# Kernel tuning notes

Hardware: AMD Instinct MI355X
Metric: run time of the kernel (lower is better)

Reference implementation:

```python
import jax, jax.numpy as jnp
import numpy as np
import math

D_MODEL = 1024
NHEAD = 16
D_K = D_MODEL // NHEAD
LAMDA_ATT = 1.0
B, L = 2, 2048


def setup_inputs() -> dict:
    key = jax.random.key(0)
    ks = jax.random.split(key, 10)
    s = 1.0 / math.sqrt(D_MODEL)
    x = jax.random.normal(ks[0], (B, L, D_MODEL), dtype=jnp.float32)
    delta_r = jax.random.uniform(ks[1], (B, L), dtype=jnp.float32)  # positive, fed to log
    Wq = jax.random.normal(ks[2], (D_MODEL, D_MODEL), dtype=jnp.float32) * s
    Wk = jax.random.normal(ks[3], (D_MODEL, D_MODEL), dtype=jnp.float32) * s
    Wv = jax.random.normal(ks[4], (D_MODEL, D_MODEL), dtype=jnp.float32) * s
    Wo = jax.random.normal(ks[5], (D_MODEL, D_MODEL), dtype=jnp.float32) * s
    bq = jnp.zeros((D_MODEL,), jnp.float32)
    bk = jnp.zeros((D_MODEL,), jnp.float32)
    bv = jnp.zeros((D_MODEL,), jnp.float32)
    bo = jnp.zeros((D_MODEL,), jnp.float32)
    return {"x": x, "delta_r": delta_r, "Wq": Wq, "bq": bq, "Wk": Wk, "bk": bk,
            "Wv": Wv, "bv": bv, "Wo": Wo, "bo": bo}


def reference(x, delta_r, Wq, bq, Wk, bk, Wv, bv, Wo, bo):
    b, l, d = x.shape
    h, dk = NHEAD, D_K

    def proj(y, W, bias):
        # [B,L,D] -> [B,H,L,dk]
        return (y @ W + bias).reshape(b, l, h, dk).transpose(0, 2, 1, 3)

    v_scaled = x * delta_r[..., None]
    q = proj(x, Wq, bq)
    k = proj(x, Wk, bk)
    v = proj(v_scaled, Wv, bv)

    scores = jnp.einsum('bhqd,bhkd->bhqk', q, k) / math.sqrt(dk)
    pos = jnp.arange(l)
    dist = jnp.abs(pos[None, :] - pos[:, None]).astype(scores.dtype)  # [L,L]
    rel_bias = LAMDA_ATT * jnp.log(delta_r + 1e-6)  # [B,L]
    scores = scores - dist[None, None] * 0.1 + rel_bias[:, None, None, :]

    attn = jax.nn.softmax(scores, axis=-1)  # dropout is identity in eval mode
    context = jnp.einsum('bhqk,bhkd->bqhd', attn, v).reshape(b, l, d)
    out = context @ Wo + bo
    return out, attn.mean(axis=1)
```

## Files before the change

### kernel.cpp

```cpp
#include <hip/hip_runtime.h>
#include <math.h>

#define DMODEL 1024
#define NHEAD  16
#define DK     64
#define BB     2
#define LL     2048
#define MTOT   (BB*LL)

#define LOG2E      1.4426950408889634f
#define SCQ        (0.125f * LOG2E)
#define C2LOG      (0.1f * LOG2E)
#define SKIP_BOUND (-24.0f)

typedef __bf16 bf16_t;
typedef __bf16 bf16x8 __attribute__((ext_vector_type(8)));
typedef __bf16 bf16x4 __attribute__((ext_vector_type(4)));
typedef float  f32x4  __attribute__((ext_vector_type(4)));

static __device__ __forceinline__ f32x4 mfma16(bf16x8 a, bf16x8 b, f32x4 c) {
    return __builtin_amdgcn_mfma_f32_16x16x32_bf16(a, b, c, 0, 0, 0);
}
static __device__ __forceinline__ float exp2f_fast(float x) {
    return __builtin_amdgcn_exp2f(x);
}
static __device__ __forceinline__ float log2f_fast(float x) {
    return __builtin_amdgcn_logf(x);
}
static __device__ __forceinline__ void gl_lds16(const bf16_t* g, bf16_t* l) {
    __builtin_amdgcn_global_load_lds(
        (const __attribute__((address_space(1))) unsigned int*)g,
        (__attribute__((address_space(3))) unsigned int*)l, 16, 0, 0);
}

__global__ __launch_bounds__(256) void prep_fused_k(
    const float* __restrict__ x, const float* __restrict__ dr,
    bf16_t* __restrict__ xb, float* __restrict__ logd2,
    const float* __restrict__ Wq, const float* __restrict__ Wk,
    const float* __restrict__ Wv, const float* __restrict__ Wo,
    bf16_t* __restrict__ Wcat, bf16_t* __restrict__ Wot)
{
    __shared__ __align__(16) float Ts[64][68];
    const int bid = blockIdx.x;
    const int tid = threadIdx.x;
    if (bid < 2048) {
        size_t gid = (size_t)bid * 256 + tid;
        size_t off = gid * 8;
        float4 a = *(const float4*)(x + off);
        float4 c = *(const float4*)(x + off + 4);
        float va[8] = {a.x, a.y, a.z, a.w, c.x, c.y, c.z, c.w};
        bf16x8 o1;
#pragma unroll
        for (int j = 0; j < 8; ++j) o1[j] = (bf16_t)va[j];
        *(bf16x8*)(xb + off) = o1;
        if (gid < MTOT) logd2[gid] = log2f_fast(dr[gid] + 1e-6f);
    } else {
        const int t = bid - 2048;
        const int z = t >> 8;
        const float* W = (z == 0) ? Wq : (z == 1) ? Wk : (z == 2) ? Wv : Wo;
        bf16_t* dst = (z < 3) ? (Wcat + (size_t)z * DMODEL * DMODEL) : Wot;
        const int k0 = (t & 15) * 64, n0 = ((t >> 4) & 15) * 64;
#pragma unroll
        for (int i = 0; i < 4; ++i) {
            int u = tid + 256 * i, r = u >> 4, c4 = (u & 15) * 4;
            *(float4*)&Ts[r][c4] = *(const float4*)(W + (size_t)(k0 + r) * DMODEL + n0 + c4);
        }
        __syncthreads();
#pragma unroll
        for (int i = 0; i < 2; ++i) {
            int u = tid + 256 * i, n = u >> 3, k8 = (u & 7) * 8;
            bf16x8 v;
#pragma unroll
            for (int j = 0; j < 8; ++j) v[j] = (bf16_t)Ts[k8 + j][n];
            *(bf16x8*)(dst + (size_t)(n0 + n) * DMODEL + k0 + k8) = v;
        }
    }
}

__global__ __launch_bounds__(256, 3) void gemm128_k(
    const bf16_t* __restrict__ A, const bf16_t* __restrict__ Bt,
    const float* __restrict__ b0, const float* __restrict__ b1,
    const float* __restrict__ b2, const float* __restrict__ delta,
    float* __restrict__ outf, bf16_t* __restrict__ outQ,
    bf16_t* __restrict__ outK, bf16_t* __restrict__ outVt, int mode)
{
    __shared__ __align__(16) bf16_t Asw[128 * 64];
    __shared__ __align__(16) bf16_t Bsw[128 * 64];
    const int tid = threadIdx.x, lane = tid & 63, w = tid >> 6;
    const int quad = lane >> 4, n16 = lane & 15;
    const int wm = (w & 1) * 64, wn = (w >> 1) * 64;
    const int m0 = blockIdx.y * 128, n0 = blockIdx.x * 128;
    const int srow = lane >> 3;
    const int scb  = (lane & 7) ^ srow;

    f32x4 acc[4][4] = {};

    for (int K0 = 0; K0 < DMODEL; K0 += 64) {
        __syncthreads();
#pragma unroll
        for (int i = 0; i < 4; ++i) {
            int rb = w * 32 + i * 8;
            gl_lds16(A  + (size_t)(m0 + rb + srow) * DMODEL + K0 + scb * 8,
                     &Asw[rb * 64]);
            gl_lds16(Bt + (size_t)(n0 + rb + srow) * DMODEL + K0 + scb * 8,
                     &Bsw[rb * 64]);
        }
        __syncthreads();
#pragma unroll
        for (int kc = 0; kc < 2; ++kc) {
            const int pcb = ((kc * 4 + quad) ^ (n16 & 7)) * 8;
            bf16x8 af[4], bfv[4];
#pragma unroll
            for (int mi = 0; mi < 4; ++mi)
                af[mi] = *(const bf16x8*)&Asw[(wm + mi * 16 + n16) * 64 + pcb];
#pragma unroll
            for (int ni = 0; ni < 4; ++ni)
                bfv[ni] = *(const bf16x8*)&Bsw[(wn + ni * 16 + n16) * 64 + pcb];
#pragma unroll
            for (int mi = 0; mi < 4; ++mi)
#pragma unroll
                for (int ni = 0; ni < 4; ++ni)
                    acc[mi][ni] = mfma16(af[mi], bfv[ni], acc[mi][ni]);
        }
    }

    if (mode == 0) {
        const int region = n0 >> 10;
        if (region == 2) {
#pragma unroll
            for (int mi = 0; mi < 4; ++mi) {
                const int mbase = m0 + wm + mi * 16 + quad * 4;
                const int bidx = mbase >> 11, l = mbase & (LL - 1);
                const f32x4 dm4 = *(const f32x4*)(delta + mbase);
#pragma unroll
                for (int ni = 0; ni < 4; ++ni) {
                    const int nl = (n0 & 1023) + wn + ni * 16 + n16;
                    const int h = nl >> 6, dd = nl & 63;
                    const float bv = b2[nl];
                    bf16x4 pk;
#pragma unroll
                    for (int r = 0; r < 4; ++r)
                        pk[r] = (bf16_t)(acc[mi][ni][r] * dm4[r] + bv);
                    *(bf16x4*)(outVt + ((size_t)(bidx * NHEAD + h) * DK + dd) * LL + l) = pk;
                }
            }
        } else {
            const float* bias = (region == 0) ? b0 : b1;
            bf16_t* dst = (region == 0) ? outQ : outK;
            const float qs = (region == 0) ? SCQ : 1.0f;
#pragma unroll
            for (int mi = 0; mi < 4; ++mi) {
#pragma unroll
                for (int r = 0; r < 4; ++r) {
                    const int m = m0 + wm + mi * 16 + quad * 4 + r;
                    const int bidx = m >> 11, l = m & (LL - 1);
#pragma unroll
                    for (int ni = 0; ni < 4; ++ni) {
                        const int nl = (n0 & 1023) + wn + ni * 16 + n16;
                        const int h = nl >> 6, dd = nl & 63;
                        float v = (acc[mi][ni][r] + bias[nl]) * qs;
                        dst[(((size_t)(bidx * NHEAD + h) * LL) + l) * DK + dd] = (bf16_t)v;
                    }
                }
            }
        }
    } else {
#pragma unroll
        for (int mi = 0; mi < 4; ++mi) {
#pragma unroll
            for (int r = 0; r < 4; ++r) {
                const int m = m0 + wm + mi * 16 + quad * 4 + r;
#pragma unroll
                for (int ni = 0; ni < 4; ++ni) {
                    const int n = n0 + wn + ni * 16 + n16;
                    outf[(size_t)m * DMODEL + n] = acc[mi][ni][r] + b0[n];
                }
            }
        }
    }
}

__global__ __launch_bounds__(256) void stats_k(
    const bf16_t* __restrict__ Q, const bf16_t* __restrict__ K,
    const float* __restrict__ logd2, float* __restrict__ Qn,
    float* __restrict__ Kn, float* __restrict__ dlb, float* __restrict__ ldx)
{
    __shared__ float qn_s[2048], kn_s[2048], dg_s[2048];
    const int tid = threadIdx.x, bh = blockIdx.x, b = bh >> 4;
    const size_t base = (size_t)bh * LL * DK;
#pragma unroll
    for (int i = 0; i < 8; ++i) {
        const int row = tid + 256 * i;
        float qn2 = 0.f, kn2 = 0.f, dg = 0.f;
#pragma unroll
        for (int j = 0; j < 8; ++j) {
            bf16x8 qv = *(const bf16x8*)(Q + base + (size_t)row * DK + j * 8);
            bf16x8 kv = *(const bf16x8*)(K + base + (size_t)row * DK + j * 8);
#pragma unroll
            for (int e = 0; e < 8; ++e) {
                float fq = (float)qv[e], fk = (float)kv[e];
                qn2 += fq * fq; kn2 += fk * fk; dg += fq * fk;
            }
        }
        qn_s[row] = qn2;
        kn_s[row] = kn2;
        dg_s[row] = dg + logd2[b * LL + row];
    }
    __syncthreads();
    if (tid < 16) {
        float mq = 0.f, md = 1e30f;
        for (int r = 0; r < 128; ++r) {
            mq = fmaxf(mq, qn_s[tid * 128 + r]);
            md = fminf(md, dg_s[tid * 128 + r]);
        }
        Qn[bh * 16 + tid] = sqrtf(mq);
        dlb[bh * 16 + tid] = md;
    } else if (tid >= 64 && tid < 96) {
        const int t = tid - 64;
        float mk = 0.f;
        for (int r = 0; r < 64; ++r) mk = fmaxf(mk, kn_s[t * 64 + r]);
        Kn[bh * 32 + t] = sqrtf(mk);
    } else if (tid >= 128 && tid < 160 && (bh & 15) == 0) {
        const int t = tid - 128;
        float ml = -1e30f;
        for (int r = 0; r < 64; ++r) ml = fmaxf(ml, logd2[b * LL + t * 64 + r]);
        ldx[b * 32 + t] = ml;
    }
}

__global__ __launch_bounds__(256) void mlstat_k(
    const float* __restrict__ mlws, float* __restrict__ mlmin)
{
    __shared__ float s[2048];
    const int tid = threadIdx.x, bh = blockIdx.x;
#pragma unroll
    for (int i = 0; i < 8; ++i)
        s[tid + 256 * i] = mlws[(size_t)bh * LL + tid + 256 * i];
    __syncthreads();
    if (tid < 16) {
        float m = 1e30f;
        for (int r = 0; r < 128; ++r) m = fminf(m, s[tid * 128 + r]);
        mlmin[bh * 16 + tid] = m;
    }
}

__global__ __launch_bounds__(256, 4) void attn_flash_mfma_k(
    const bf16_t* __restrict__ Q, const bf16_t* __restrict__ K,
    const bf16_t* __restrict__ Vt, const float* __restrict__ logd2,
    const float* __restrict__ Qn, const float* __restrict__ Kn,
    const float* __restrict__ dlb, const float* __restrict__ ldx,
    bf16_t* __restrict__ ctx, float* __restrict__ mlout)
{
    __shared__ __align__(16) bf16_t Ks[64][72];
    __shared__ __align__(16) bf16_t Vts[64][72];
    __shared__ __align__(16) bf16_t Ps[4][16][72];
    __shared__ float logds[64];

    const int tid = threadIdx.x;
    const int lane = tid & 63, w = tid >> 6;
    const int quad = lane >> 4, n16 = lane & 15;
    const int bh = blockIdx.x, b = bh >> 4, h = bh & 15;
    const int qt = blockIdx.y, q0 = qt * 64;
    const size_t base = (size_t)bh * LL * DK;
    const int q = q0 + w * 16 + n16;

    bf16x8 qa[2];
#pragma unroll
    for (int kc = 0; kc < 2; ++kc)
        qa[kc] = *(const bf16x8*)(Q + base + (size_t)q * DK + kc * 32 + quad * 8);

    unsigned mask = 0;
    {
        const float qn = Qn[bh * 16 + (qt >> 1)], dl = dlb[bh * 16 + (qt >> 1)];
        for (int t = 0; t < 32; ++t) {
            const int kc0 = t * 64;
            const int dmin = (kc0 > q0 + 63) ? (kc0 - (q0 + 63))
                           : ((q0 > kc0 + 63) ? (q0 - (kc0 + 63)) : 0);
            const float bound = qn * Kn[bh * 32 + t] + ldx[b * 32 + t]
                              - C2LOG * (float)dmin - dl;
            if (bound > SKIP_BOUND) mask |= (1u << t);
        }
    }

    const int strow = tid >> 3, stc8 = (tid & 7) * 8;
    bf16x8 kr0, kr1, vr0, vr1;
    float ldr = 0.f;
    auto prefetch = [&](int k0) {
        kr0 = *(const bf16x8*)(K + base + (size_t)(k0 + strow) * DK + stc8);
        kr1 = *(const bf16x8*)(K + base + (size_t)(k0 + 32 + strow) * DK + stc8);
        vr0 = *(const bf16x8*)(Vt + base + (size_t)strow * LL + k0 + stc8);
        vr1 = *(const bf16x8*)(Vt + base + (size_t)(32 + strow) * LL + k0 + stc8);
        if (tid < 64) ldr = logd2[b * LL + k0 + tid];
    };

    float m_c = -1e30f, l_c = 0.f;
    f32x4 o[4] = {};
    const float dfq = (float)(q - quad * 4);

    int t = (int)__builtin_ctz(mask);
    prefetch(t * 64);
    for (;;) {
        const unsigned rem = (t < 31) ? (mask >> (t + 1)) : 0u;
        const int tn = rem ? (t + 1 + (int)__builtin_ctz(rem)) : -1;
        __syncthreads();
        *(bf16x8*)&Ks[strow][stc8]       = kr0;
        *(bf16x8*)&Ks[32 + strow][stc8]  = kr1;
        *(bf16x8*)&Vts[strow][stc8]      = vr0;
        *(bf16x8*)&Vts[32 + strow][stc8] = vr1;
        if (tid < 64) logds[tid] = ldr;
        __syncthreads();
        if (tn >= 0) prefetch(tn * 64);
        const int k0 = t * 64;

        f32x4 s[4] = {};
#pragma unroll
        for (int kc = 0; kc < 2; ++kc) {
#pragma unroll
            for (int kt = 0; kt < 4; ++kt) {
                bf16x8 kb = *(const bf16x8*)&Ks[kt * 16 + n16][kc * 32 + quad * 8];
                s[kt] = mfma16(kb, qa[kc], s[kt]);
            }
        }
        const float df = dfq - (float)k0;
#pragma unroll
        for (int kt = 0; kt < 4; ++kt) {
            f32x4 ldv = *(const f32x4*)&logds[kt * 16 + quad * 4];
#pragma unroll
            for (int r = 0; r < 4; ++r)
                s[kt][r] += ldv[r] - C2LOG * fabsf(df - (float)(kt * 16 + r));
        }
        f32x4 mx;
#pragma unroll
        for (int r = 0; r < 4; ++r)
            mx[r] = fmaxf(fmaxf(s[0][r], s[1][r]), fmaxf(s[2][r], s[3][r]));
        float rm = fmaxf(fmaxf(mx[0], mx[1]), fmaxf(mx[2], mx[3]));
        rm = fmaxf(rm, __shfl_xor(rm, 16));
        rm = fmaxf(rm, __shfl_xor(rm, 32));
        const float mn = fmaxf(m_c, rm);
        const float alpha = exp2f_fast(m_c - mn);
        if (__any(mn > m_c)) {
#pragma unroll
            for (int dt = 0; dt < 4; ++dt)
#pragma unroll
                for (int r = 0; r < 4; ++r) o[dt][r] *= alpha;
        }
        f32x4 ps = {0.f, 0.f, 0.f, 0.f};
#pragma unroll
        for (int kt = 0; kt < 4; ++kt)
#pragma unroll
            for (int r = 0; r < 4; ++r) {
                float p = exp2f_fast(s[kt][r] - mn);
                s[kt][r] = p;
                ps[r] += p;
            }
        float psum = (ps[0] + ps[1]) + (ps[2] + ps[3]);
        psum += __shfl_xor(psum, 16);
        psum += __shfl_xor(psum, 32);
        l_c = l_c * alpha + psum;
        m_c = mn;
#pragma unroll
        for (int kt = 0; kt < 4; ++kt) {
            bf16x4 pk;
#pragma unroll
            for (int r = 0; r < 4; ++r) pk[r] = (bf16_t)s[kt][r];
            *(bf16x4*)&Ps[w][n16][kt * 16 + quad * 4] = pk;
        }
        __threadfence_block();
#pragma unroll
        for (int kc = 0; kc < 2; ++kc) {
            bf16x8 pa = *(const bf16x8*)&Ps[w][n16][kc * 32 + quad * 8];
#pragma unroll
            for (int dt = 0; dt < 4; ++dt) {
                bf16x8 vb = *(const bf16x8*)&Vts[dt * 16 + n16][kc * 32 + quad * 8];
                o[dt] = mfma16(vb, pa, o[dt]);
            }
        }
        if (tn < 0) break;
        t = tn;
    }
    const float inv = 1.f / l_c;
#pragma unroll
    for (int dt = 0; dt < 4; ++dt) {
        bf16x4 ov;
#pragma unroll
        for (int r = 0; r < 4; ++r) ov[r] = (bf16_t)(o[dt][r] * inv);
        *(bf16x4*)(ctx + ((size_t)b * LL + q) * DMODEL + h * DK +
                   dt * 16 + quad * 4) = ov;
    }
    if (quad == 0)
        mlout[(size_t)bh * LL + q] = m_c + log2f_fast(l_c);
}

__global__ __launch_bounds__(256, 3) void tail_fused_k(
    const bf16_t* __restrict__ A, const bf16_t* __restrict__ Bt,
    const float* __restrict__ b0, float* __restrict__ outf,
    const bf16_t* __restrict__ Q, const bf16_t* __restrict__ K,
    const float* __restrict__ logd2, const float* __restrict__ mlws,
    const float* __restrict__ Qn, const float* __restrict__ Kn,
    const float* __restrict__ mlmin, const float* __restrict__ ldx,
    float* __restrict__ outmean)
{
    __shared__ __align__(16) bf16_t Asw[64 * 64];
    __shared__ __align__(16) bf16_t Bsw[128 * 64];
    __shared__ __align__(16) bf16_t Ks[2][64][72];
    __shared__ float mls[2][128];
    __shared__ float logds[64];

    const int bid = blockIdx.x;
    const int tid = threadIdx.x;
    const int lane = tid & 63, w = tid >> 6;
    const int quad = lane >> 4, n16 = lane & 15;

    if (bid < 512) {
        const int wm = (w & 1) * 32, wn = (w >> 1) * 64;
        const int m0 = (bid >> 3) * 64, n0 = (bid & 7) * 128;
        const int srow = lane >> 3;
        const int scb  = (lane & 7) ^ srow;

        f32x4 acc[2][4] = {};

        for (int K0 = 0; K0 < DMODEL; K0 += 64) {
            __syncthreads();
#pragma unroll
            for (int i = 0; i < 2; ++i) {
                int rb = w * 16 + i * 8;
                gl_lds16(A + (size_t)(m0 + rb + srow) * DMODEL + K0 + scb * 8,
                         &Asw[rb * 64]);
            }
#pragma unroll
            for (int i = 0; i < 4; ++i) {
                int rb = w * 32 + i * 8;
                gl_lds16(Bt + (size_t)(n0 + rb + srow) * DMODEL + K0 + scb * 8,
                         &Bsw[rb * 64]);
            }
            __syncthreads();
#pragma unroll
            for (int kc = 0; kc < 2; ++kc) {
                const int pcb = ((kc * 4 + quad) ^ (n16 & 7)) * 8;
                bf16x8 af[2], bfv[4];
#pragma unroll
                for (int mi = 0; mi < 2; ++mi)
                    af[mi] = *(const bf16x8*)&Asw[(wm + mi * 16 + n16) * 64 + pcb];
#pragma unroll
                for (int ni = 0; ni < 4; ++ni)
                    bfv[ni] = *(const bf16x8*)&Bsw[(wn + ni * 16 + n16) * 64 + pcb];
#pragma unroll
                for (int mi = 0; mi < 2; ++mi)
#pragma unroll
                    for (int ni = 0; ni < 4; ++ni)
                        acc[mi][ni] = mfma16(af[mi], bfv[ni], acc[mi][ni]);
            }
        }
#pragma unroll
        for (int mi = 0; mi < 2; ++mi) {
#pragma unroll
            for (int r = 0; r < 4; ++r) {
                const int m = m0 + wm + mi * 16 + quad * 4 + r;
#pragma unroll
                for (int ni = 0; ni < 4; ++ni) {
                    const int n = n0 + wn + ni * 16 + n16;
                    outf[(size_t)m * DMODEL + n] = acc[mi][ni][r] + b0[n];
                }
            }
        }
        return;
    }

    const int tb = bid - 512;
    const int k0 = (tb & 31) * 64, q0 = ((tb >> 5) & 15) * 128, b = tb >> 9;
    const int qq[2] = {q0 + w * 32 + n16, q0 + w * 32 + 16 + n16};

    if (tid < 64) logds[tid] = logd2[b * LL + k0 + tid];
    __syncthreads();

    float bias0[2][4][4];
#pragma unroll
    for (int qg = 0; qg < 2; ++qg) {
        const float df = (float)(qq[qg] - k0 - quad * 4);
#pragma unroll
        for (int kt = 0; kt < 4; ++kt) {
            f32x4 ldv = *(const f32x4*)&logds[kt * 16 + quad * 4];
#pragma unroll
            for (int r = 0; r < 4; ++r)
                bias0[qg][kt][r] = ldv[r] - C2LOG * fabsf(df - (float)(kt * 16 + r));
        }
    }

    const int qt = q0 >> 7, ktl = k0 >> 6;
    const int dmin = (k0 > q0 + 127) ? (k0 - (q0 + 127))
                   : ((q0 > k0 + 63) ? (q0 - (k0 + 63)) : 0);
    unsigned hmask = 0;
    {
        const float dterm = ldx[b * 32 + ktl] - C2LOG * (float)dmin;
        for (int h = 0; h < NHEAD; ++h) {
            const int bh = b * 16 + h;
            const float bound = Qn[bh * 16 + qt] * Kn[bh * 32 + ktl] + dterm
                              - mlmin[bh * 16 + qt];
            if (bound > SKIP_BOUND) hmask |= (1u << h);
        }
    }

    f32x4 acc[2][4] = {};

    if (hmask) {
        const int strow = tid >> 3, stc8 = (tid & 7) * 8;
        bf16x8 kr0, kr1, qan[2][2];
        float mlv = 0.f;
        auto load_head = [&](int h) {
            const size_t hb = (size_t)(b * NHEAD + h) * LL * DK;
            kr0 = *(const bf16x8*)(K + hb + (size_t)(k0 + strow) * DK + stc8);
            kr1 = *(const bf16x8*)(K + hb + (size_t)(k0 + 32 + strow) * DK + stc8);
#pragma unroll
            for (int qg = 0; qg < 2; ++qg)
#pragma unroll
                for (int kc = 0; kc < 2; ++kc)
                    qan[qg][kc] = *(const bf16x8*)(Q + hb + (size_t)qq[qg] * DK +
                                                   kc * 32 + quad * 8);
            if (tid < 128) mlv = mlws[(size_t)(b * NHEAD + h) * LL + q0 + tid];
        };

        int h = (int)__builtin_ctz(hmask);
        load_head(h);
        int pc = 0;
        for (;;) {
            const unsigned rem = (h < 15) ? (hmask >> (h + 1)) : 0u;
            const int hn = rem ? (h + 1 + (int)__builtin_ctz(rem)) : -1;
            const int p = pc & 1;
            *(bf16x8*)&Ks[p][strow][stc8]      = kr0;
            *(bf16x8*)&Ks[p][32 + strow][stc8] = kr1;
            if (tid < 128) mls[p][tid] = mlv;
            bf16x8 qc[2][2] = {{qan[0][0], qan[0][1]}, {qan[1][0], qan[1][1]}};
            __syncthreads();
            if (hn >= 0) load_head(hn);

            f32x4 s[2][4] = {};
#pragma unroll
            for (int kc = 0; kc < 2; ++kc) {
#pragma unroll
                for (int kt = 0; kt < 4; ++kt) {
                    bf16x8 kb = *(const bf16x8*)&Ks[p][kt * 16 + n16][kc * 32 + quad * 8];
                    s[0][kt] = mfma16(kb, qc[0][kc], s[0][kt]);
                    s[1][kt] = mfma16(kb, qc[1][kc], s[1][kt]);
                }
            }
#pragma unroll
            for (int qg = 0; qg < 2; ++qg) {
                const float ml = mls[p][w * 32 + qg * 16 + n16];
#pragma unroll
                for (int kt = 0; kt < 4; ++kt)
#pragma unroll
                    for (int r = 0; r < 4; ++r)
                        acc[qg][kt][r] += exp2f_fast(s[qg][kt][r] +
                                                     bias0[qg][kt][r] - ml);
            }
            ++pc;
            if (hn < 0) break;
            h = hn;
        }
    }

    const float invH = 1.f / (float)NHEAD;
#pragma unroll
    for (int qg = 0; qg < 2; ++qg)
#pragma unroll
        for (int kt = 0; kt < 4; ++kt) {
            f32x4 ov;
#pragma unroll
            for (int r = 0; r < 4; ++r) ov[r] = acc[qg][kt][r] * invH;
            *(f32x4*)(outmean + ((size_t)b * LL + qq[qg]) * LL + k0 +
                      kt * 16 + quad * 4) = ov;
        }
}

extern "C" void kernel_launch(void* const* d_in, const int* in_sizes, int n_in,
                              void* d_out, int out_size, void* d_ws, size_t ws_size,
                              hipStream_t stream) {
    const float* x  = (const float*)d_in[0];
    const float* dr = (const float*)d_in[1];
    const float* Wq = (const float*)d_in[2];
    const float* bq = (const float*)d_in[3];
    const float* Wk = (const float*)d_in[4];
    const float* bk = (const float*)d_in[5];
    const float* Wv = (const float*)d_in[6];
    const float* bv = (const float*)d_in[7];
    const float* Wo = (const float*)d_in[8];
    const float* bo = (const float*)d_in[9];
    float* out = (float*)d_out;
    char* ws = (char*)d_ws;
    const size_t MB = 1ull << 20;

    bf16_t* xb   = (bf16_t*)(ws);
    bf16_t* Wcat = (bf16_t*)(ws + 8 * MB);
    bf16_t* Wot  = (bf16_t*)(ws + 14 * MB);
    bf16_t* Qb   = (bf16_t*)(ws + 16 * MB);
    bf16_t* Kb   = (bf16_t*)(ws + 24 * MB);
    bf16_t* Vtb  = (bf16_t*)(ws + 32 * MB);
    float*  logd = (float*)(ws + 40 * MB);
    float*  mlws = (float*)(ws + 41 * MB);
    float*  Qns  = (float*)(ws + 42 * MB);
    float*  Kns  = (float*)(ws + 42 * MB + 4096);
    float*  dlb  = (float*)(ws + 42 * MB + 12288);
    float*  ldxp = (float*)(ws + 42 * MB + 16384);
    float*  mlmn = (float*)(ws + 42 * MB + 20480);
    bf16_t* ctx  = xb;

    prep_fused_k<<<3072, 256, 0, stream>>>(x, dr, xb, logd,
                                           Wq, Wk, Wv, Wo, Wcat, Wot);

    gemm128_k<<<dim3(24, 32), 256, 0, stream>>>(xb, Wcat, bq, bk, bv, dr,
                                                nullptr, Qb, Kb, Vtb, 0);
    stats_k<<<32, 256, 0, stream>>>(Qb, Kb, logd, Qns, Kns, dlb, ldxp);

    attn_flash_mfma_k<<<dim3(32, 32), 256, 0, stream>>>(Qb, Kb, Vtb, logd,
                                                        Qns, Kns, dlb, ldxp,
                                                        ctx, mlws);
    mlstat_k<<<32, 256, 0, stream>>>(mlws, mlmn);
    tail_fused_k<<<1536, 256, 0, stream>>>(ctx, Wot, bo, out,
                                           Qb, Kb, logd, mlws, Qns, Kns,
                                           mlmn, ldxp,
                                           out + (size_t)MTOT * DMODEL);
}
```

Baseline: 238.0 us.

## Split stats kernel across more blocks and alias tail kernel shared memory

The stats kernel now launches 256 blocks, each covering one 256-row segment of a batch-head, instead of 32 blocks looping over 2048 rows. This spreads the bandwidth-bound norm reductions over far more CUs. The tail fused kernel also overlays its GEMM and attention-mean shared buffers in one union-like char array, cutting LDS per block so more blocks can be resident. The risk is smaller per-block work and correct offsets in the aliased LDS layout.

```diff
diff --git a/kernel.cpp b/kernel.cpp
--- a/kernel.cpp
+++ b/kernel.cpp
@@ -185,46 +185,48 @@
     const float* __restrict__ logd2, float* __restrict__ Qn,
     float* __restrict__ Kn, float* __restrict__ dlb, float* __restrict__ ldx)
 {
-    __shared__ float qn_s[2048], kn_s[2048], dg_s[2048];
-    const int tid = threadIdx.x, bh = blockIdx.x, b = bh >> 4;
+    __shared__ float qn_s[256], kn_s[256], dg_s[256];
+    const int blk = blockIdx.x;
+    const int bh = blk >> 3, seg = blk & 7, b = bh >> 4;
+    const int tid = threadIdx.x;
+    const int row = seg * 256 + tid;
     const size_t base = (size_t)bh * LL * DK;
-#pragma unroll
-    for (int i = 0; i < 8; ++i) {
-        const int row = tid + 256 * i;
-        float qn2 = 0.f, kn2 = 0.f, dg = 0.f;
-#pragma unroll
-        for (int j = 0; j < 8; ++j) {
-            bf16x8 qv = *(const bf16x8*)(Q + base + (size_t)row * DK + j * 8);
-            bf16x8 kv = *(const bf16x8*)(K + base + (size_t)row * DK + j * 8);
-#pragma unroll
-            for (int e = 0; e < 8; ++e) {
-                float fq = (float)qv[e], fk = (float)kv[e];
-                qn2 += fq * fq; kn2 += fk * fk; dg += fq * fk;
-            }
-        }
-        qn_s[row] = qn2;
-        kn_s[row] = kn2;
-        dg_s[row] = dg + logd2[b * LL + row];
-    }
+
+    float qn2 = 0.f, kn2 = 0.f, dg = 0.f;
+#pragma unroll
+    for (int j = 0; j < 8; ++j) {
+        bf16x8 qv = *(const bf16x8*)(Q + base + (size_t)row * DK + j * 8);
+        bf16x8 kv = *(const bf16x8*)(K + base + (size_t)row * DK + j * 8);
+#pragma unroll
+        for (int e = 0; e < 8; ++e) {
+            float fq = (float)qv[e], fk = (float)kv[e];
+            qn2 += fq * fq; kn2 += fk * fk; dg += fq * fk;
+        }
+    }
+    qn_s[tid] = qn2;
+    kn_s[tid] = kn2;
+    dg_s[tid] = dg + logd2[b * LL + row];
     __syncthreads();
-    if (tid < 16) {
+
+    if (tid < 2) {
         float mq = 0.f, md = 1e30f;
         for (int r = 0; r < 128; ++r) {
             mq = fmaxf(mq, qn_s[tid * 128 + r]);
             md = fminf(md, dg_s[tid * 128 + r]);
         }
-        Qn[bh * 16 + tid] = sqrtf(mq);
-        dlb[bh * 16 + tid] = md;
-    } else if (tid >= 64 && tid < 96) {
+        Qn[bh * 16 + seg * 2 + tid] = sqrtf(mq);
+        dlb[bh * 16 + seg * 2 + tid] = md;
+    } else if (tid >= 64 && tid < 68) {
         const int t = tid - 64;
         float mk = 0.f;
         for (int r = 0; r < 64; ++r) mk = fmaxf(mk, kn_s[t * 64 + r]);
-        Kn[bh * 32 + t] = sqrtf(mk);
-    } else if (tid >= 128 && tid < 160 && (bh & 15) == 0) {
+        Kn[bh * 32 + seg * 4 + t] = sqrtf(mk);
+    } else if (tid >= 128 && tid < 132 && (bh & 15) == 0) {
         const int t = tid - 128;
         float ml = -1e30f;
-        for (int r = 0; r < 64; ++r) ml = fmaxf(ml, logd2[b * LL + t * 64 + r]);
-        ldx[b * 32 + t] = ml;
+        for (int r = 0; r < 64; ++r)
+            ml = fmaxf(ml, logd2[b * LL + seg * 256 + t * 64 + r]);
+        ldx[b * 32 + seg * 4 + t] = ml;
     }
 }
 
@@ -400,11 +402,7 @@
     const float* __restrict__ mlmin, const float* __restrict__ ldx,
     float* __restrict__ outmean)
 {
-    __shared__ __align__(16) bf16_t Asw[64 * 64];
-    __shared__ __align__(16) bf16_t Bsw[128 * 64];
-    __shared__ __align__(16) bf16_t Ks[2][64][72];
-    __shared__ float mls[2][128];
-    __shared__ float logds[64];
+    __shared__ __align__(16) char smem[24576];
 
     const int bid = blockIdx.x;
     const int tid = threadIdx.x;
@@ -412,6 +410,8 @@
     const int quad = lane >> 4, n16 = lane & 15;
 
     if (bid < 512) {
+        bf16_t* Asw = (bf16_t*)smem;
+        bf16_t* Bsw = (bf16_t*)(smem + 8192);
         const int wm = (w & 1) * 32, wn = (w >> 1) * 64;
         const int m0 = (bid >> 3) * 64, n0 = (bid & 7) * 128;
         const int srow = lane >> 3;
@@ -465,6 +465,11 @@
         }
         return;
     }
+
+    typedef bf16_t KsRow[64][72];
+    KsRow* Ks = (KsRow*)smem;
+    float (*mls)[128] = (float(*)[128])(smem + 18432);
+    float* logds = (float*)(smem + 19456);
 
     const int tb = bid - 512;
     const int k0 = (tb & 31) * 64, q0 = ((tb >> 5) & 15) * 128, b = tb >> 9;
@@ -609,7 +614,7 @@
 
     gemm128_k<<<dim3(24, 32), 256, 0, stream>>>(xb, Wcat, bq, bk, bv, dr,
                                                 nullptr, Qb, Kb, Vtb, 0);
-    stats_k<<<32, 256, 0, stream>>>(Qb, Kb, logd, Qns, Kns, dlb, ldxp);
+    stats_k<<<256, 256, 0, stream>>>(Qb, Kb, logd, Qns, Kns, dlb, ldxp);
 
     attn_flash_mfma_k<<<dim3(32, 32), 256, 0, stream>>>(Qb, Kb, Vtb, logd,
                                                         Qns, Kns, dlb, ldxp,
```

New measurement: 219.6 us. -7.8%, faster.
